# Kernel tuning notes

Hardware: AMD Instinct MI355X
Metric: run time of the kernel (lower is better)

## Reference

```python
import jax, jax.numpy as jnp
import numpy as np


def setup_inputs() -> dict:
    key = jax.random.key(0)
    k1, k2 = jax.random.split(key)
    x = jax.random.normal(k1, (8, 2048, 1024), dtype=jnp.float32)
    kernel = jax.random.normal(k2, (3, 1024, 1024), dtype=jnp.float32) * 0.02
    return {"x": x, "kernel": kernel}


def reference(x, kernel):
    # x: [b, s, d]; kernel: [3, d, o]
    q = jnp.einsum('bsd,do->bso', x, kernel[0])
    k = jnp.einsum('bsd,do->bso', x, kernel[1])
    v = jnp.einsum('bsd,do->bso', x, kernel[2])
    seq_len = x.shape[1]
    # NOTE: original scales by sqrt(seq_len), not sqrt(d_k)
    scores = jnp.einsum('bqo,bko->bqk', q, k) / (seq_len ** 0.5)
    attn = jax.nn.softmax(scores, axis=-1)
    return jnp.einsum('bqk,bko->bqo', attn, v)
```

## Files before the change

### kernel.cpp

```cpp
#include <hip/hip_runtime.h>
#include <stdint.h>

typedef __bf16  bf16x8  __attribute__((ext_vector_type(8)));
typedef float   f32x4   __attribute__((ext_vector_type(4)));
typedef unsigned short ushort8 __attribute__((ext_vector_type(8)));
typedef unsigned short ushort4v __attribute__((ext_vector_type(4)));

#define DEV __device__ __forceinline__

DEV unsigned short f2bf(float f) {
    union { float f; unsigned u; } v; v.f = f;
    unsigned u = v.u;
    return (unsigned short)((u + 0x7FFFu + ((u >> 16) & 1u)) >> 16);
}
DEV float bf2f(unsigned short h) {
    union { unsigned u; float f; } v; v.u = ((unsigned)h) << 16;
    return v.f;
}

DEV void gload16(const void* g, void* l) {
    __builtin_amdgcn_global_load_lds(
        (const __attribute__((address_space(1))) unsigned int*)g,
        (__attribute__((address_space(3))) unsigned int*)l, 16, 0, 0);
}

template<bool OUT_BF16>
__global__ __launch_bounds__(512, 2)
void gemm256(const unsigned short* __restrict__ A, long lda, long sA,
             const unsigned short* __restrict__ B, long ldb, long sB,
             void* __restrict__ Cv, long ldc, long sC,
             int N, int K, float alpha)
{
    __shared__ __attribute__((aligned(16))) char sm[131072];

    const int bz = blockIdx.z;
    A += (long)bz * sA;
    B += (long)bz * sB;

    const int tiles_n = N >> 8;
    int bid = blockIdx.x;
    const int nwg = gridDim.x;
    {
        const int q = nwg >> 3, r = nwg & 7;
        const int xcd = bid & 7, idx = bid >> 3;
        bid = (xcd < r ? xcd * (q + 1) : r * (q + 1) + (xcd - r) * q) + idx;
    }
    const long brow = (long)(bid / tiles_n) << 8;
    const long bcol = (long)(bid % tiles_n) << 8;

    const int t = threadIdx.x;
    const int w = t >> 6, lane = t & 63;
    const int wr = w >> 2, wc = w & 3;
    const int lr = lane & 15, lk = lane >> 4;

    const int srow = (w << 3) + (lane >> 3);
    const int scol = ((lane & 7) ^ (lane >> 3)) << 3;
    const unsigned short* gA = A + (brow + srow) * lda + scol;
    const unsigned short* gB = B + (bcol + srow) * ldb + scol;
    char* const dstA = sm + w * 1024;
    char* const dstB = sm + 32768 + w * 1024;

    const int rsw0 = ((lk ^ (lr & 7)) << 4);
    const int aoff = wr * 16384 + lr * 128;
    const int boff = 32768 + (wc >> 1) * 16384 + (((wc & 1) << 6) + lr) * 128;

    f32x4 acc[8][4];
#pragma unroll
    for (int m = 0; m < 8; ++m)
#pragma unroll
        for (int n = 0; n < 4; ++n) acc[m][n] = 0.f;

    const int nk = K >> 6;

#define STAGE_A(buf, half, kt) { \
    const unsigned short* s_ = gA + (long)((half) * 128) * lda + (long)(kt) * 64; \
    char* d_ = dstA + (buf) * 65536 + (half) * 16384; \
    gload16(s_, d_); gload16(s_ + 64 * lda, d_ + 8192); }
#define STAGE_B(buf, half, kt) { \
    const unsigned short* s_ = gB + (long)((half) * 128) * ldb + (long)(kt) * 64; \
    char* d_ = dstB + (buf) * 65536 + (half) * 16384; \
    gload16(s_, d_); gload16(s_ + 64 * ldb, d_ + 8192); }

    STAGE_A(0, 0, 0); STAGE_A(0, 1, 0); STAGE_B(0, 0, 0); STAGE_B(0, 1, 0);
    if (nk > 1) {
        STAGE_A(1, 0, 1); STAGE_A(1, 1, 1);
        asm volatile("s_waitcnt vmcnt(4)" ::: "memory");
    } else {
        asm volatile("s_waitcnt vmcnt(0)" ::: "memory");
    }
    __builtin_amdgcn_s_barrier();

    for (int kt = 0; kt < nk; ++kt) {
        const int buf = kt & 1;
        const char* sa = sm + buf * 65536 + aoff;
        const char* sb = sm + buf * 65536 + boff;
        bf16x8 a[8][2], b[4][2];

#pragma unroll
        for (int m = 0; m < 4; ++m) {
            a[m][0] = *(const bf16x8*)(sa + m * 2048 + rsw0);
            a[m][1] = *(const bf16x8*)(sa + m * 2048 + (rsw0 ^ 64));
        }
#pragma unroll
        for (int n = 0; n < 2; ++n) {
            b[n][0] = *(const bf16x8*)(sb + n * 2048 + rsw0);
            b[n][1] = *(const bf16x8*)(sb + n * 2048 + (rsw0 ^ 64));
        }
        if (kt + 1 < nk) STAGE_B(buf ^ 1, 0, kt + 1);
        __builtin_amdgcn_s_barrier();
        __builtin_amdgcn_s_setprio(1);
#pragma unroll
        for (int m = 0; m < 4; ++m)
#pragma unroll
            for (int n = 0; n < 2; ++n)
#pragma unroll
                for (int ks = 0; ks < 2; ++ks)
                    acc[m][n] = __builtin_amdgcn_mfma_f32_16x16x32_bf16(
                        a[m][ks], b[n][ks], acc[m][n], 0, 0, 0);
        __builtin_amdgcn_s_setprio(0);
        __builtin_amdgcn_s_barrier();

#pragma unroll
        for (int m = 4; m < 8; ++m) {
            a[m][0] = *(const bf16x8*)(sa + m * 2048 + rsw0);
            a[m][1] = *(const bf16x8*)(sa + m * 2048 + (rsw0 ^ 64));
        }
#pragma unroll
        for (int n = 2; n < 4; ++n) {
            b[n][0] = *(const bf16x8*)(sb + n * 2048 + rsw0);
            b[n][1] = *(const bf16x8*)(sb + n * 2048 + (rsw0 ^ 64));
        }
        if (kt + 1 < nk) STAGE_B(buf ^ 1, 1, kt + 1);
        __builtin_amdgcn_s_barrier();
        __builtin_amdgcn_s_setprio(1);
#pragma unroll
        for (int m = 0; m < 4; ++m)
#pragma unroll
            for (int n = 2; n < 4; ++n)
#pragma unroll
                for (int ks = 0; ks < 2; ++ks)
                    acc[m][n] = __builtin_amdgcn_mfma_f32_16x16x32_bf16(
                        a[m][ks], b[n][ks], acc[m][n], 0, 0, 0);
        __builtin_amdgcn_s_setprio(0);
        asm volatile("s_waitcnt lgkmcnt(0)" ::: "memory");
        __builtin_amdgcn_s_barrier();

        if (kt + 2 < nk) STAGE_A(buf, 0, kt + 2);
        __builtin_amdgcn_s_setprio(1);
#pragma unroll
        for (int m = 4; m < 8; ++m)
#pragma unroll
            for (int n = 0; n < 2; ++n)
#pragma unroll
                for (int ks = 0; ks < 2; ++ks)
                    acc[m][n] = __builtin_amdgcn_mfma_f32_16x16x32_bf16(
                        a[m][ks], b[n][ks], acc[m][n], 0, 0, 0);
        __builtin_amdgcn_s_setprio(0);
        __builtin_amdgcn_s_barrier();

        if (kt + 2 < nk) {
            STAGE_A(buf, 1, kt + 2);
            asm volatile("s_waitcnt vmcnt(4)" ::: "memory");
        } else if (kt + 1 < nk) {
            asm volatile("s_waitcnt vmcnt(0)" ::: "memory");
        }
        __builtin_amdgcn_s_setprio(1);
#pragma unroll
        for (int m = 4; m < 8; ++m)
#pragma unroll
            for (int n = 2; n < 4; ++n)
#pragma unroll
                for (int ks = 0; ks < 2; ++ks)
                    acc[m][n] = __builtin_amdgcn_mfma_f32_16x16x32_bf16(
                        a[m][ks], b[n][ks], acc[m][n], 0, 0, 0);
        __builtin_amdgcn_s_setprio(0);
        __builtin_amdgcn_s_barrier();
    }
#undef STAGE_A
#undef STAGE_B

    const long r0 = brow + wr * 128;
    const long c0 = bcol + wc * 64;
    if (OUT_BF16) {
        unsigned short* C = (unsigned short*)Cv + (long)bz * sC;
#pragma unroll
        for (int m = 0; m < 8; ++m)
#pragma unroll
            for (int n = 0; n < 4; ++n) {
                const long c = c0 + n * 16 + lr;
#pragma unroll
                for (int j = 0; j < 4; ++j) {
                    const long r = r0 + m * 16 + lk * 4 + j;
                    C[r * ldc + c] = f2bf(acc[m][n][j] * alpha);
                }
            }
    } else {
        float* C = (float*)Cv + (long)bz * sC;
#pragma unroll
        for (int m = 0; m < 8; ++m)
#pragma unroll
            for (int n = 0; n < 4; ++n) {
                const long c = c0 + n * 16 + lr;
#pragma unroll
                for (int j = 0; j < 4; ++j) {
                    const long r = r0 + m * 16 + lk * 4 + j;
                    C[r * ldc + c] = acc[m][n][j] * alpha;
                }
            }
    }
}

__global__ __launch_bounds__(256)
void conv_x(const f32x4* __restrict__ X, ushort4v* __restrict__ Y, long n4)
{
    long i = (long)blockIdx.x * 256 + threadIdx.x;
    const long stride = (long)gridDim.x * 256;
    for (; i < n4; i += stride) {
        f32x4 v = X[i];
        ushort4v o;
#pragma unroll
        for (int j = 0; j < 4; ++j) o[j] = f2bf(v[j]);
        Y[i] = o;
    }
}

__global__ __launch_bounds__(256)
void conv_w(const float* __restrict__ W, unsigned short* __restrict__ Wt)
{
    __shared__ unsigned short tile[64][65];
    const long hofs = (long)blockIdx.z * 1048576;
    const int d0 = blockIdx.x * 64;
    const int o0 = blockIdx.y * 64;
    const int t = threadIdx.x;
    const int c  = t & 63;
    const int r0 = t >> 6;
#pragma unroll
    for (int rr = 0; rr < 64; rr += 4) {
        const int r = rr + r0;
        tile[r][c] = f2bf(W[hofs + (long)(d0 + r) * 1024 + (o0 + c)]);
    }
    __syncthreads();
#pragma unroll
    for (int rr = 0; rr < 64; rr += 4) {
        const int r = rr + r0;
        Wt[hofs + (long)(o0 + r) * 1024 + (d0 + c)] = tile[c][r];
    }
}

__global__ __launch_bounds__(256)
void softmax_rows(unsigned short* __restrict__ P)
{
    __shared__ float red[4];
    unsigned short* p = P + (long)blockIdx.x * 2048;
    const int t = threadIdx.x;
    const int lane = t & 63, wave = t >> 6;

    ushort8 u = *(const ushort8*)(p + t * 8);
    float x[8];
    float mx = -3.0e38f;
#pragma unroll
    for (int j = 0; j < 8; ++j) { x[j] = bf2f(u[j]); mx = fmaxf(mx, x[j]); }
#pragma unroll
    for (int o = 1; o < 64; o <<= 1) mx = fmaxf(mx, __shfl_xor(mx, o));
    if (lane == 0) red[wave] = mx;
    __syncthreads();
    mx = fmaxf(fmaxf(red[0], red[1]), fmaxf(red[2], red[3]));
    __syncthreads();

    float e[8], s = 0.f;
#pragma unroll
    for (int j = 0; j < 8; ++j) { e[j] = __expf(x[j] - mx); s += e[j]; }
#pragma unroll
    for (int o = 1; o < 64; o <<= 1) s += __shfl_xor(s, o);
    if (lane == 0) red[wave] = s;
    __syncthreads();
    s = red[0] + red[1] + red[2] + red[3];

    const float inv = 1.0f / s;
    ushort8 o8;
#pragma unroll
    for (int j = 0; j < 8; ++j) o8[j] = f2bf(e[j] * inv);
    *(ushort8*)(p + t * 8) = o8;
}

extern "C" void kernel_launch(void* const* d_in, const int* in_sizes, int n_in,
                              void* d_out, int out_size, void* d_ws, size_t ws_size,
                              hipStream_t stream)
{
    const float* x = (const float*)d_in[0];
    const float* w = (const float*)d_in[1];
    float* out = (float*)d_out;

    const long BS = 16384;
    const long D  = 1024;
    const long S  = 2048;

    char* ws = (char*)d_ws;
    unsigned short* Xb = (unsigned short*)ws; ws += BS * D * 2;
    unsigned short* Wt = (unsigned short*)ws; ws += 3L * D * D * 2;
    unsigned short* QK = (unsigned short*)ws; ws += BS * 2 * D * 2;
    unsigned short* Vt = (unsigned short*)ws; ws += D * BS * 2;
    unsigned short* P  = (unsigned short*)ws; ws += 8L * S * S * 2;

    conv_x<<<4096, 256, 0, stream>>>((const f32x4*)x, (ushort4v*)Xb, BS * D / 4);
    conv_w<<<dim3(16, 16, 3), 256, 0, stream>>>(w, Wt);

    gemm256<true><<<dim3((BS / 256) * (2048 / 256), 1, 1), 512, 0, stream>>>(
        Xb, D, 0, Wt, D, 0, QK, 2 * D, 0, 2048, (int)D, 1.f);

    gemm256<true><<<dim3((1024 / 256) * (BS / 256), 1, 1), 512, 0, stream>>>(
        Wt + 2L * D * D, D, 0, Xb, D, 0, Vt, BS, 0, (int)BS, (int)D, 1.f);

    gemm256<true><<<dim3((S / 256) * (S / 256), 1, 8), 512, 0, stream>>>(
        QK, 2 * D, S * 2 * D,
        QK + D, 2 * D, S * 2 * D,
        P, S, S * S,
        (int)S, (int)D, 0.022097086912079612f);

    softmax_rows<<<16384, 256, 0, stream>>>(P);

    gemm256<false><<<dim3((S / 256) * (1024 / 256), 1, 8), 512, 0, stream>>>(
        P, S, S * S,
        Vt, BS, S,
        out, D, S * D,
        1024, (int)S, 1.f);
}
```

Before: 388.9 us.

## Restructure GEMM main loop fragment loads and batch softmax rows per block

The GEMM main loop now splits its A/B fragments into separate register sets, loads only the needed halves in each phase, and reorders the MFMA loops so ks is outermost. Global-pointer increments replace per-iteration address recomputation, and the explicit lgkmcnt(0) wait before the third phase is removed. Separately, the softmax kernel processes 8 rows per block with 2048 blocks instead of one row per block, which adds an extra barrier per row. Together these aim to cut LDS-load stalls, address arithmetic, and launch/scheduling overhead, at the cost of possible register-pressure changes and lower softmax parallelism.

```diff
diff --git a/kernel.cpp b/kernel.cpp
--- a/kernel.cpp
+++ b/kernel.cpp
@@ -59,6 +59,8 @@
     const unsigned short* gB = B + (bcol + srow) * ldb + scol;
     char* const dstA = sm + w * 1024;
     char* const dstB = sm + 32768 + w * 1024;
+    const long lda64 = 64 * lda, ldaH = 128 * lda;
+    const long ldb64 = 64 * ldb, ldbH = 128 * ldb;
 
     const int rsw0 = ((lk ^ (lr & 7)) << 4);
     const int aoff = wr * 16384 + lr * 128;
@@ -72,112 +74,130 @@
 
     const int nk = K >> 6;
 
-#define STAGE_A(buf, half, kt) { \
-    const unsigned short* s_ = gA + (long)((half) * 128) * lda + (long)(kt) * 64; \
-    char* d_ = dstA + (buf) * 65536 + (half) * 16384; \
-    gload16(s_, d_); gload16(s_ + 64 * lda, d_ + 8192); }
-#define STAGE_B(buf, half, kt) { \
-    const unsigned short* s_ = gB + (long)((half) * 128) * ldb + (long)(kt) * 64; \
-    char* d_ = dstB + (buf) * 65536 + (half) * 16384; \
-    gload16(s_, d_); gload16(s_ + 64 * ldb, d_ + 8192); }
-
-    STAGE_A(0, 0, 0); STAGE_A(0, 1, 0); STAGE_B(0, 0, 0); STAGE_B(0, 1, 0);
+    gload16(gA,                dstA);
+    gload16(gA + lda64,        dstA + 8192);
+    gload16(gA + ldaH,         dstA + 16384);
+    gload16(gA + ldaH + lda64, dstA + 16384 + 8192);
+    gload16(gB,                dstB);
+    gload16(gB + ldb64,        dstB + 8192);
+    gload16(gB + ldbH,         dstB + 16384);
+    gload16(gB + ldbH + ldb64, dstB + 16384 + 8192);
     if (nk > 1) {
-        STAGE_A(1, 0, 1); STAGE_A(1, 1, 1);
+        gload16(gA + 64,                dstA + 65536);
+        gload16(gA + 64 + lda64,        dstA + 65536 + 8192);
+        gload16(gA + 64 + ldaH,         dstA + 65536 + 16384);
+        gload16(gA + 64 + ldaH + lda64, dstA + 65536 + 16384 + 8192);
         asm volatile("s_waitcnt vmcnt(4)" ::: "memory");
     } else {
         asm volatile("s_waitcnt vmcnt(0)" ::: "memory");
     }
     __builtin_amdgcn_s_barrier();
+
+    const unsigned short* gAk = gA;
+    const unsigned short* gBk = gB;
 
     for (int kt = 0; kt < nk; ++kt) {
         const int buf = kt & 1;
         const char* sa = sm + buf * 65536 + aoff;
         const char* sb = sm + buf * 65536 + boff;
-        bf16x8 a[8][2], b[4][2];
+        char* const dA = dstA + buf * 65536;
+        char* const dB = dstB + (buf ^ 1) * 65536;
+        bf16x8 a0[4][2], a1[4][2], b01[2][2], b23[2][2];
 
 #pragma unroll
         for (int m = 0; m < 4; ++m) {
-            a[m][0] = *(const bf16x8*)(sa + m * 2048 + rsw0);
-            a[m][1] = *(const bf16x8*)(sa + m * 2048 + (rsw0 ^ 64));
+            a0[m][0] = *(const bf16x8*)(sa + m * 2048 + rsw0);
+            a0[m][1] = *(const bf16x8*)(sa + m * 2048 + (rsw0 ^ 64));
         }
 #pragma unroll
         for (int n = 0; n < 2; ++n) {
-            b[n][0] = *(const bf16x8*)(sb + n * 2048 + rsw0);
-            b[n][1] = *(const bf16x8*)(sb + n * 2048 + (rsw0 ^ 64));
-        }
-        if (kt + 1 < nk) STAGE_B(buf ^ 1, 0, kt + 1);
+            b01[n][0] = *(const bf16x8*)(sb + n * 2048 + rsw0);
+            b01[n][1] = *(const bf16x8*)(sb + n * 2048 + (rsw0 ^ 64));
+        }
+        if (kt + 1 < nk) {
+            gload16(gBk + 64,         dB);
+            gload16(gBk + 64 + ldb64, dB + 8192);
+        }
         __builtin_amdgcn_s_barrier();
         __builtin_amdgcn_s_setprio(1);
 #pragma unroll
-        for (int m = 0; m < 4; ++m)
-#pragma unroll
-            for (int n = 0; n < 2; ++n)
-#pragma unroll
-                for (int ks = 0; ks < 2; ++ks)
+        for (int ks = 0; ks < 2; ++ks)
+#pragma unroll
+            for (int m = 0; m < 4; ++m)
+#pragma unroll
+                for (int n = 0; n < 2; ++n)
                     acc[m][n] = __builtin_amdgcn_mfma_f32_16x16x32_bf16(
-                        a[m][ks], b[n][ks], acc[m][n], 0, 0, 0);
+                        a0[m][ks], b01[n][ks], acc[m][n], 0, 0, 0);
         __builtin_amdgcn_s_setprio(0);
         __builtin_amdgcn_s_barrier();
 
 #pragma unroll
-        for (int m = 4; m < 8; ++m) {
-            a[m][0] = *(const bf16x8*)(sa + m * 2048 + rsw0);
-            a[m][1] = *(const bf16x8*)(sa + m * 2048 + (rsw0 ^ 64));
-        }
-#pragma unroll
-        for (int n = 2; n < 4; ++n) {
-            b[n][0] = *(const bf16x8*)(sb + n * 2048 + rsw0);
-            b[n][1] = *(const bf16x8*)(sb + n * 2048 + (rsw0 ^ 64));
-        }
-        if (kt + 1 < nk) STAGE_B(buf ^ 1, 1, kt + 1);
+        for (int n = 0; n < 2; ++n) {
+            b23[n][0] = *(const bf16x8*)(sb + (n + 2) * 2048 + rsw0);
+            b23[n][1] = *(const bf16x8*)(sb + (n + 2) * 2048 + (rsw0 ^ 64));
+        }
+        if (kt + 1 < nk) {
+            gload16(gBk + 64 + ldbH,         dB + 16384);
+            gload16(gBk + 64 + ldbH + ldb64, dB + 16384 + 8192);
+        }
         __builtin_amdgcn_s_barrier();
         __builtin_amdgcn_s_setprio(1);
 #pragma unroll
-        for (int m = 0; m < 4; ++m)
-#pragma unroll
-            for (int n = 2; n < 4; ++n)
-#pragma unroll
-                for (int ks = 0; ks < 2; ++ks)
-                    acc[m][n] = __builtin_amdgcn_mfma_f32_16x16x32_bf16(
-                        a[m][ks], b[n][ks], acc[m][n], 0, 0, 0);
+        for (int ks = 0; ks < 2; ++ks)
+#pragma unroll
+            for (int m = 0; m < 4; ++m)
+#pragma unroll
+                for (int n = 0; n < 2; ++n)
+                    acc[m][n + 2] = __builtin_amdgcn_mfma_f32_16x16x32_bf16(
+                        a0[m][ks], b23[n][ks], acc[m][n + 2], 0, 0, 0);
         __builtin_amdgcn_s_setprio(0);
-        asm volatile("s_waitcnt lgkmcnt(0)" ::: "memory");
-        __builtin_amdgcn_s_barrier();
-
-        if (kt + 2 < nk) STAGE_A(buf, 0, kt + 2);
+        __builtin_amdgcn_s_barrier();
+
+#pragma unroll
+        for (int m = 0; m < 4; ++m) {
+            a1[m][0] = *(const bf16x8*)(sa + (m + 4) * 2048 + rsw0);
+            a1[m][1] = *(const bf16x8*)(sa + (m + 4) * 2048 + (rsw0 ^ 64));
+        }
+        if (kt + 2 < nk) {
+            gload16(gAk + 128,         dA);
+            gload16(gAk + 128 + lda64, dA + 8192);
+        }
+        __builtin_amdgcn_s_barrier();
         __builtin_amdgcn_s_setprio(1);
 #pragma unroll
-        for (int m = 4; m < 8; ++m)
-#pragma unroll
-            for (int n = 0; n < 2; ++n)
-#pragma unroll
-                for (int ks = 0; ks < 2; ++ks)
-                    acc[m][n] = __builtin_amdgcn_mfma_f32_16x16x32_bf16(
-                        a[m][ks], b[n][ks], acc[m][n], 0, 0, 0);
+        for (int ks = 0; ks < 2; ++ks)
+#pragma unroll
+            for (int m = 0; m < 4; ++m)
+#pragma unroll
+                for (int n = 0; n < 2; ++n)
+                    acc[m + 4][n] = __builtin_amdgcn_mfma_f32_16x16x32_bf16(
+                        a1[m][ks], b01[n][ks], acc[m + 4][n], 0, 0, 0);
         __builtin_amdgcn_s_setprio(0);
         __builtin_amdgcn_s_barrier();
 
         if (kt + 2 < nk) {
-            STAGE_A(buf, 1, kt + 2);
+            gload16(gAk + 128 + ldaH,         dA + 16384);
+            gload16(gAk + 128 + ldaH + lda64, dA + 16384 + 8192);
+        }
+        __builtin_amdgcn_s_setprio(1);
+#pragma unroll
+        for (int ks = 0; ks < 2; ++ks)
+#pragma unroll
+            for (int m = 0; m < 4; ++m)
+#pragma unroll
+                for (int n = 0; n < 2; ++n)
+                    acc[m + 4][n + 2] = __builtin_amdgcn_mfma_f32_16x16x32_bf16(
+                        a1[m][ks], b23[n][ks], acc[m + 4][n + 2], 0, 0, 0);
+        __builtin_amdgcn_s_setprio(0);
+        if (kt + 2 < nk) {
             asm volatile("s_waitcnt vmcnt(4)" ::: "memory");
         } else if (kt + 1 < nk) {
             asm volatile("s_waitcnt vmcnt(0)" ::: "memory");
         }
-        __builtin_amdgcn_s_setprio(1);
-#pragma unroll
-        for (int m = 4; m < 8; ++m)
-#pragma unroll
-            for (int n = 2; n < 4; ++n)
-#pragma unroll
-                for (int ks = 0; ks < 2; ++ks)
-                    acc[m][n] = __builtin_amdgcn_mfma_f32_16x16x32_bf16(
-                        a[m][ks], b[n][ks], acc[m][n], 0, 0, 0);
-        __builtin_amdgcn_s_setprio(0);
-        __builtin_amdgcn_s_barrier();
-    }
-#undef STAGE_A
-#undef STAGE_B
+        __builtin_amdgcn_s_barrier();
+
+        gAk += 64; gBk += 64;
+    }
 
     const long r0 = brow + wr * 128;
     const long c0 = bcol + wc * 64;
@@ -251,36 +271,39 @@
 void softmax_rows(unsigned short* __restrict__ P)
 {
     __shared__ float red[4];
-    unsigned short* p = P + (long)blockIdx.x * 2048;
     const int t = threadIdx.x;
     const int lane = t & 63, wave = t >> 6;
 
-    ushort8 u = *(const ushort8*)(p + t * 8);
-    float x[8];
-    float mx = -3.0e38f;
-#pragma unroll
-    for (int j = 0; j < 8; ++j) { x[j] = bf2f(u[j]); mx = fmaxf(mx, x[j]); }
-#pragma unroll
-    for (int o = 1; o < 64; o <<= 1) mx = fmaxf(mx, __shfl_xor(mx, o));
-    if (lane == 0) red[wave] = mx;
-    __syncthreads();
-    mx = fmaxf(fmaxf(red[0], red[1]), fmaxf(red[2], red[3]));
-    __syncthreads();
-
-    float e[8], s = 0.f;
-#pragma unroll
-    for (int j = 0; j < 8; ++j) { e[j] = __expf(x[j] - mx); s += e[j]; }
-#pragma unroll
-    for (int o = 1; o < 64; o <<= 1) s += __shfl_xor(s, o);
-    if (lane == 0) red[wave] = s;
-    __syncthreads();
-    s = red[0] + red[1] + red[2] + red[3];
-
-    const float inv = 1.0f / s;
-    ushort8 o8;
-#pragma unroll
-    for (int j = 0; j < 8; ++j) o8[j] = f2bf(e[j] * inv);
-    *(ushort8*)(p + t * 8) = o8;
+    for (int r = 0; r < 8; ++r) {
+        unsigned short* p = P + ((long)blockIdx.x * 8 + r) * 2048;
+        ushort8 u = *(const ushort8*)(p + t * 8);
+        float x[8];
+        float mx = -3.0e38f;
+#pragma unroll
+        for (int j = 0; j < 8; ++j) { x[j] = bf2f(u[j]); mx = fmaxf(mx, x[j]); }
+#pragma unroll
+        for (int o = 1; o < 64; o <<= 1) mx = fmaxf(mx, __shfl_xor(mx, o));
+        if (lane == 0) red[wave] = mx;
+        __syncthreads();
+        mx = fmaxf(fmaxf(red[0], red[1]), fmaxf(red[2], red[3]));
+        __syncthreads();
+
+        float e[8], s = 0.f;
+#pragma unroll
+        for (int j = 0; j < 8; ++j) { e[j] = __expf(x[j] - mx); s += e[j]; }
+#pragma unroll
+        for (int o = 1; o < 64; o <<= 1) s += __shfl_xor(s, o);
+        if (lane == 0) red[wave] = s;
+        __syncthreads();
+        s = red[0] + red[1] + red[2] + red[3];
+        __syncthreads();
+
+        const float inv = 1.0f / s;
+        ushort8 o8;
+#pragma unroll
+        for (int j = 0; j < 8; ++j) o8[j] = f2bf(e[j] * inv);
+        *(ushort8*)(p + t * 8) = o8;
+    }
 }
 
 extern "C" void kernel_launch(void* const* d_in, const int* in_sizes, int n_in,
@@ -317,7 +340,7 @@
         P, S, S * S,
         (int)S, (int)D, 0.022097086912079612f);
 
-    softmax_rows<<<16384, 256, 0, stream>>>(P);
+    softmax_rows<<<2048, 256, 0, stream>>>(P);
 
     gemm256<false><<<dim3((S / 256) * (1024 / 256), 1, 8), 512, 0, stream>>>(
         P, S, S * S,
```

New measurement: 389.6 us. No clear change (+0.2%).
